# Kernel optimization log

Measured on AMD Instinct MI355X. Metric: run time of the kernel, lower is better.

The kernel has to match this reference:

```python
import jax, jax.numpy as jnp
import numpy as np

EPS = 1e-6
NUM_ITERS = 3


def rmsnorm(x, w, eps=EPS):
    # Qwen3RMSNorm: x * rsqrt(mean(x^2) + eps) * weight
    return x * jax.lax.rsqrt(jnp.mean(x * x, axis=-1, keepdims=True) + eps) * w


def setup_inputs() -> dict:
    key = jax.random.key(0)
    ks = jax.random.split(key, 12)
    B, K, M, d = 8, 64, 4096, 1024
    s = 0.02  # keep projections at sane init scale
    return {
        "slots": jax.random.normal(ks[0], (B, K, d), jnp.float32),
        "P": jax.random.normal(ks[1], (B, M, d), jnp.float32),
        "Wq": jax.random.normal(ks[2], (d, d), jnp.float32) * s,
        "Wk": jax.random.normal(ks[3], (d, d), jnp.float32) * s,
        "Wv": jax.random.normal(ks[4], (d, d), jnp.float32) * s,
        "gru_wi": jax.random.normal(ks[5], (3 * d, d), jnp.float32) * s,
        "gru_wh": jax.random.normal(ks[6], (3 * d, d), jnp.float32) * s,
        "gru_bi": jax.random.normal(ks[7], (3 * d,), jnp.float32) * s,
        "gru_bh": jax.random.normal(ks[8], (3 * d,), jnp.float32) * s,
        "slot_norm_w": jnp.ones((d,), jnp.float32),
        "input_norm_w": jnp.ones((d,), jnp.float32),
    }


def gru_cell(x, h, wi, wh, bi, bh):
    # PyTorch nn.GRUCell semantics; x,h: (..., d)
    d = h.shape[-1]
    gi = jnp.einsum('...d,ed->...e', x, wi) + bi  # (..., 3d)
    gh = jnp.einsum('...d,ed->...e', h, wh) + bh
    ir, iz, inn = gi[..., :d], gi[..., d:2 * d], gi[..., 2 * d:]
    hr, hz, hn = gh[..., :d], gh[..., d:2 * d], gh[..., 2 * d:]
    r = jax.nn.sigmoid(ir + hr)
    z = jax.nn.sigmoid(iz + hz)
    n = jnp.tanh(inn + r * hn)
    return (1.0 - z) * n + z * h


def reference(slots, P, Wq, Wk, Wv, gru_wi, gru_wh, gru_bi, gru_bh,
              slot_norm_w, input_norm_w):
    d = slots.shape[-1]
    scale = d ** (-0.5)
    Pn = rmsnorm(P, input_norm_w)
    k_proj = jnp.einsum('bmd,ed->bme', Pn, Wk)  # Linear: x @ W.T
    v_proj = jnp.einsum('bmd,ed->bme', Pn, Wv)
    for _ in range(NUM_ITERS):
        sn = rmsnorm(slots, slot_norm_w)
        q = jnp.einsum('bkd,ed->bke', sn, Wq)
        scores = jnp.einsum('bkd,bmd->bkm', q, k_proj) * scale
        attn = jax.nn.softmax(scores, axis=-2)  # softmax over SLOT axis K
        attn = attn / (jnp.sum(attn, axis=-1, keepdims=True) + EPS)
        updates = jnp.einsum('bkm,bmd->bkd', attn, v_proj)
        slots = gru_cell(updates, slots, gru_wi, gru_wh, gru_bi, gru_bh)
    return slots
```

## Files before the change

### kernel.cpp

```cpp
#include <hip/hip_runtime.h>

typedef __attribute__((ext_vector_type(4))) float f32x4;
typedef __attribute__((ext_vector_type(8))) short s16x8;

static __device__ __forceinline__ unsigned short f2bf(float f) {
  unsigned int u = __builtin_bit_cast(unsigned int, f);
  u += 0x7fffu + ((u >> 16) & 1u);
  return (unsigned short)(u >> 16);
}
static __device__ __forceinline__ float bf2f(unsigned short u) {
  return __builtin_bit_cast(float, (unsigned int)u << 16);
}
static __device__ __forceinline__ float sigm(float x) { return 1.0f / (1.0f + __expf(-x)); }

static __device__ __forceinline__ void gload16(const unsigned short* g, unsigned short* l) {
  __builtin_amdgcn_global_load_lds(
      (const __attribute__((address_space(1))) void*)g,
      (__attribute__((address_space(3))) void*)l, 16, 0, 0);
}

__global__ __launch_bounds__(256) void rmsnorm_k(const float* __restrict__ x,
                                                 const float* __restrict__ w,
                                                 unsigned short* __restrict__ y,
                                                 unsigned short* __restrict__ y_raw) {
  const int row = blockIdx.x;
  const int tid = threadIdx.x;
  const float4* xp = (const float4*)(x + (long)row * 1024);
  float4 v = xp[tid];
  float ss = v.x * v.x + v.y * v.y + v.z * v.z + v.w * v.w;
  #pragma unroll
  for (int off = 32; off; off >>= 1) ss += __shfl_xor(ss, off, 64);
  __shared__ float sb[4];
  if ((tid & 63) == 0) sb[tid >> 6] = ss;
  __syncthreads();
  float tot = sb[0] + sb[1] + sb[2] + sb[3];
  float rs = rsqrtf(tot * (1.0f / 1024.0f) + 1e-6f);
  const float4* wp = (const float4*)w;
  float4 wv = wp[tid];
  ushort4 o;
  o.x = f2bf(v.x * rs * wv.x);
  o.y = f2bf(v.y * rs * wv.y);
  o.z = f2bf(v.z * rs * wv.z);
  o.w = f2bf(v.w * rs * wv.w);
  ((ushort4*)y)[(long)row * 256 + tid] = o;
  if (y_raw) {
    ushort4 r;
    r.x = f2bf(v.x); r.y = f2bf(v.y); r.z = f2bf(v.z); r.w = f2bf(v.w);
    ((ushort4*)y_raw)[(long)row * 256 + tid] = r;
  }
}

__global__ __launch_bounds__(256) void tp_k(const unsigned short* __restrict__ in,
                                            unsigned short* __restrict__ out) {
  __shared__ unsigned short t[64][65];
  const int x = blockIdx.x;
  const int b = x >> 10;
  const int mt = (x & 1023) >> 4;
  const int dt = x & 15;
  const int tid = threadIdx.x;
  const long ibase = (long)b * 4096 * 1024 + (long)mt * 64 * 1024 + dt * 64;
  #pragma unroll
  for (int i = 0; i < 4; i++) {
    int idx = tid + i * 256;
    int r = idx >> 4, c4 = (idx & 15) * 4;
    ushort4 v = *(const ushort4*)(in + ibase + (long)r * 1024 + c4);
    t[r][c4] = v.x; t[r][c4 + 1] = v.y; t[r][c4 + 2] = v.z; t[r][c4 + 3] = v.w;
  }
  __syncthreads();
  const long obase = (long)b * 1024 * 4096 + (long)dt * 64 * 4096 + mt * 64;
  #pragma unroll
  for (int i = 0; i < 4; i++) {
    int idx = tid + i * 256;
    int r = idx >> 4, c4 = (idx & 15) * 4;
    ushort4 o;
    o.x = t[c4][r]; o.y = t[c4 + 1][r]; o.z = t[c4 + 2][r]; o.w = t[c4 + 3][r];
    *(ushort4*)(out + obase + (long)r * 4096 + c4) = o;
  }
}

static __device__ __forceinline__ void cvt_chunk(const float* __restrict__ in,
                                                 unsigned short* __restrict__ out, long i) {
  const float4* p = (const float4*)in;
  float4 a = p[i * 2], b = p[i * 2 + 1];
  ushort4 lo, hi;
  lo.x = f2bf(a.x); lo.y = f2bf(a.y); lo.z = f2bf(a.z); lo.w = f2bf(a.w);
  hi.x = f2bf(b.x); hi.y = f2bf(b.y); hi.z = f2bf(b.z); hi.w = f2bf(b.w);
  ushort4* o = (ushort4*)out;
  o[i * 2] = lo;
  o[i * 2 + 1] = hi;
}

__global__ __launch_bounds__(256) void prep_k(
    const float* __restrict__ Wq, const float* __restrict__ Wk, const float* __restrict__ Wv,
    const float* __restrict__ wi, const float* __restrict__ wh,
    const float* __restrict__ slots_in, const float* __restrict__ snw,
    unsigned short* __restrict__ wqt, unsigned short* __restrict__ wkt,
    unsigned short* __restrict__ wvt, unsigned short* __restrict__ wi_b,
    unsigned short* __restrict__ wh_b, unsigned short* __restrict__ sn,
    unsigned short* __restrict__ slotsb) {
  __shared__ float tile[64][65];
  const int x = blockIdx.x;
  const int tid = threadIdx.x;
  if (x < 768) {
    const int z = x >> 8, t = x & 255;
    const float* in = (z == 0) ? Wq : (z == 1) ? Wk : Wv;
    unsigned short* out = (z == 0) ? wqt : (z == 1) ? wkt : wvt;
    const int r0 = (t >> 4) * 64, c0 = (t & 15) * 64;
    #pragma unroll
    for (int i = 0; i < 4; i++) {
      int idx = tid + i * 256;
      int r = idx >> 4, c4 = (idx & 15) * 4;
      float4 v = *(const float4*)(in + (long)(r0 + r) * 1024 + c0 + c4);
      tile[r][c4] = v.x; tile[r][c4 + 1] = v.y; tile[r][c4 + 2] = v.z; tile[r][c4 + 3] = v.w;
    }
    __syncthreads();
    #pragma unroll
    for (int i = 0; i < 4; i++) {
      int idx = tid + i * 256;
      int c = idx >> 4, r4 = (idx & 15) * 4;
      ushort4 o;
      o.x = f2bf(tile[r4][c]);     o.y = f2bf(tile[r4 + 1][c]);
      o.z = f2bf(tile[r4 + 2][c]); o.w = f2bf(tile[r4 + 3][c]);
      *(ushort4*)(out + (long)(c0 + c) * 1024 + r0 + r4) = o;
    }
  } else if (x < 3840) {
    const int y = x - 768;
    if (y < 1536) cvt_chunk(wi, wi_b, (long)y * 256 + tid);
    else          cvt_chunk(wh, wh_b, (long)(y - 1536) * 256 + tid);
  } else {
    const int row = x - 3840;
    const float4* xp = (const float4*)(slots_in + (long)row * 1024);
    float4 v = xp[tid];
    float ss = v.x * v.x + v.y * v.y + v.z * v.z + v.w * v.w;
    #pragma unroll
    for (int off = 32; off; off >>= 1) ss += __shfl_xor(ss, off, 64);
    float* sb = &tile[0][0];
    if ((tid & 63) == 0) sb[tid >> 6] = ss;
    __syncthreads();
    float tot = sb[0] + sb[1] + sb[2] + sb[3];
    float rs = rsqrtf(tot * (1.0f / 1024.0f) + 1e-6f);
    float4 wv = ((const float4*)snw)[tid];
    ushort4 o;
    o.x = f2bf(v.x * rs * wv.x); o.y = f2bf(v.y * rs * wv.y);
    o.z = f2bf(v.z * rs * wv.z); o.w = f2bf(v.w * rs * wv.w);
    ((ushort4*)sn)[(long)row * 256 + tid] = o;
    ushort4 r;
    r.x = f2bf(v.x); r.y = f2bf(v.y); r.z = f2bf(v.z); r.w = f2bf(v.w);
    ((ushort4*)slotsb)[(long)row * 256 + tid] = r;
  }
}

template <int BM, int BN, int WR, int WC, typename CT, int EPI, int SPLIT, int QGH>
__global__ __launch_bounds__(WR * WC * 64) void gemm_bt(
    const unsigned short* __restrict__ A, const unsigned short* __restrict__ W,
    CT* __restrict__ C, int N, int Klen, int lda, int ldw,
    long sA, long sW, long sC, const float* __restrict__ bias,
    const float* __restrict__ bias2, float alpha, float* __restrict__ rs_part,
    const unsigned short* __restrict__ A2, const unsigned short* __restrict__ W2) {
  constexpr int BK = 64;
  constexpr int NT = WR * WC * 64;
  static_assert(NT == 256, "256 threads");
  constexpr int WSM = BM / WR, WSN = BN / WC;
  constexpr int MR = WSM / 16, NR = WSN / 16;
  constexpr int SEG_A = BM / 8, SEG_W = BN / 8;
  constexpr int PA = SEG_A / 4, PW = SEG_W / 4;
  static_assert(SEG_A % 4 == 0 && SEG_W % 4 == 0, "seg divisibility");
  __shared__ unsigned short As[BM * BK];
  __shared__ unsigned short Ws[BN * BK];
  const int tid = threadIdx.x, lane = tid & 63, wid = tid >> 6;
  const int wr = wid / WC, wc = wid % WC;
  const int tileN = blockIdx.x * BN, tileM = blockIdx.y * BM;
  int coff = 0;
  int zb = 0;
  if constexpr (QGH) {
    const int zz = blockIdx.z;
    if (zz > 0) {
      A = A2;
      W = W2 + (long)(zz - 1) * 1024 * ldw;
      bias = bias2 + (zz - 1) * 1024;
      coff = zz * 1024;
    }
  } else {
    zb = blockIdx.z / SPLIT;
    const int zs = blockIdx.z % SPLIT;
    A += (long)zb * sA + (long)zs * Klen;
    W += (long)zb * sW + (long)zs * Klen;
    C += (long)blockIdx.z * sC;
  }
  const int srow = lane >> 3;
  const int scol = (lane & 7) * 8;
  f32x4 acc[MR][NR];
  #pragma unroll
  for (int i = 0; i < MR; i++)
    #pragma unroll
    for (int j = 0; j < NR; j++) acc[i][j] = (f32x4){0.f, 0.f, 0.f, 0.f};
  const int fr = lane & 15, fq = lane >> 4;

  for (int k0 = 0; k0 < Klen; k0 += BK) {
    #pragma unroll
    for (int p = 0; p < PA; p++) {
      int seg = wid * PA + p;
      gload16(A + (long)(tileM + seg * 8 + srow) * lda + k0 + scol, &As[seg * 512]);
    }
    #pragma unroll
    for (int p = 0; p < PW; p++) {
      int seg = wid * PW + p;
      gload16(W + (long)(tileN + seg * 8 + srow) * ldw + k0 + scol, &Ws[seg * 512]);
    }
    __syncthreads();
    #pragma unroll
    for (int kk = 0; kk < BK; kk += 32) {
      s16x8 af[MR], bf[NR];
      #pragma unroll
      for (int i = 0; i < MR; i++)
        af[i] = *(const s16x8*)(&As[(wr * WSM + i * 16 + fr) * BK + kk + fq * 8]);
      #pragma unroll
      for (int j = 0; j < NR; j++)
        bf[j] = *(const s16x8*)(&Ws[(wc * WSN + j * 16 + fr) * BK + kk + fq * 8]);
      #pragma unroll
      for (int i = 0; i < MR; i++)
        #pragma unroll
        for (int j = 0; j < NR; j++)
          acc[i][j] = __builtin_amdgcn_mfma_f32_16x16x32_bf16(af[i], bf[j], acc[i][j], 0, 0, 0);
    }
    __syncthreads();
  }

  if constexpr (EPI == 2) {
    static_assert(WR == 1 && BM == 64, "softmax epilogue needs full-M wave");
    #pragma unroll
    for (int i = 0; i < MR; i++)
      #pragma unroll
      for (int j = 0; j < NR; j++)
        #pragma unroll
        for (int q = 0; q < 4; q++) acc[i][j][q] *= alpha;
    float inv[NR];
    #pragma unroll
    for (int j = 0; j < NR; j++) {
      float mx = -1e30f;
      #pragma unroll
      for (int i = 0; i < MR; i++)
        #pragma unroll
        for (int q = 0; q < 4; q++) mx = fmaxf(mx, acc[i][j][q]);
      mx = fmaxf(mx, __shfl_xor(mx, 16, 64));
      mx = fmaxf(mx, __shfl_xor(mx, 32, 64));
      float sm = 0.f;
      #pragma unroll
      for (int i = 0; i < MR; i++)
        #pragma unroll
        for (int q = 0; q < 4; q++) {
          float e = __expf(acc[i][j][q] - mx);
          acc[i][j][q] = e;
          sm += e;
        }
      sm += __shfl_xor(sm, 16, 64);
      sm += __shfl_xor(sm, 32, 64);
      inv[j] = 1.f / sm;
    }
    float rp[MR][4];
    #pragma unroll
    for (int i = 0; i < MR; i++)
      #pragma unroll
      for (int q = 0; q < 4; q++) rp[i][q] = 0.f;
    unsigned short* Cs = (unsigned short*)C;
    #pragma unroll
    for (int i = 0; i < MR; i++)
      #pragma unroll
      for (int j = 0; j < NR; j++)
        #pragma unroll
        for (int q = 0; q < 4; q++) {
          float a = acc[i][j][q] * inv[j];
          rp[i][q] += a;
          Cs[(long)(i * 16 + fq * 4 + q) * N + tileN + wc * WSN + j * 16 + fr] = f2bf(a);
        }
    #pragma unroll
    for (int off = 1; off <= 8; off <<= 1)
      #pragma unroll
      for (int i = 0; i < MR; i++)
        #pragma unroll
        for (int q = 0; q < 4; q++) rp[i][q] += __shfl_xor(rp[i][q], off, 64);
    if (fr == 0) {
      const int rld = gridDim.x * WC;
      #pragma unroll
      for (int i = 0; i < MR; i++)
        #pragma unroll
        for (int q = 0; q < 4; q++)
          rs_part[((long)zb * 64 + i * 16 + fq * 4 + q) * rld + blockIdx.x * WC + wc] = rp[i][q];
    }
    return;
  }

  #pragma unroll
  for (int i = 0; i < MR; i++) {
    const int mbase = tileM + wr * WSM + i * 16 + fq * 4;
    #pragma unroll
    for (int j = 0; j < NR; j++) {
      const int n = tileN + wc * WSN + j * 16 + fr;
      const float bv = bias ? bias[n] : 0.f;
      #pragma unroll
      for (int q = 0; q < 4; q++) {
        float v = acc[i][j][q] * alpha + bv;
        if constexpr (sizeof(CT) == 2)
          C[(long)(mbase + q) * N + coff + n] = f2bf(v);
        else
          C[(long)(mbase + q) * N + coff + n] = v;
      }
    }
  }
}

__global__ __launch_bounds__(256) void upd_reduce_k(const unsigned short* __restrict__ part,
                                                    const float* __restrict__ rs_part,
                                                    unsigned short* __restrict__ out) {
  const int row = blockIdx.x;
  const int tid = threadIdx.x;
  float s = rs_part[(long)row * 256 + tid];
  #pragma unroll
  for (int off = 32; off; off >>= 1) s += __shfl_xor(s, off, 64);
  __shared__ float sb[4];
  if ((tid & 63) == 0) sb[tid >> 6] = s;
  __syncthreads();
  const float inv = 1.f / (sb[0] + sb[1] + sb[2] + sb[3] + 1e-6f);
  const unsigned short* base =
      part + (long)(row >> 6) * 8 * 65536 + (long)(row & 63) * 1024 + tid * 4;
  float ax = 0.f, ay = 0.f, az = 0.f, aw = 0.f;
  #pragma unroll
  for (int sp = 0; sp < 8; sp++) {
    ushort4 v = *(const ushort4*)(base + (long)sp * 65536);
    ax += bf2f(v.x); ay += bf2f(v.y); az += bf2f(v.z); aw += bf2f(v.w);
  }
  ushort4 o;
  o.x = f2bf(ax * inv); o.y = f2bf(ay * inv);
  o.z = f2bf(az * inv); o.w = f2bf(aw * inv);
  ((ushort4*)out)[(long)row * 256 + tid] = o;
}

__global__ __launch_bounds__(256) void gru_k(const unsigned short* __restrict__ gi,
                                             const unsigned short* __restrict__ qgh,
                                             const float* __restrict__ h,
                                             const float* __restrict__ snw,
                                             float* __restrict__ out,
                                             unsigned short* __restrict__ out_bf,
                                             unsigned short* __restrict__ sn_out) {
  const int r = blockIdx.x;
  const int tid = threadIdx.x;
  const int c = tid * 4;
  const unsigned short* gip = gi + (long)r * 3072;
  const unsigned short* ghp = qgh + (long)r * 4096 + 1024;
  ushort4 iru = *(const ushort4*)(gip + c);
  ushort4 izu = *(const ushort4*)(gip + 1024 + c);
  ushort4 inu = *(const ushort4*)(gip + 2048 + c);
  ushort4 hru = *(const ushort4*)(ghp + c);
  ushort4 hzu = *(const ushort4*)(ghp + 1024 + c);
  ushort4 hnu = *(const ushort4*)(ghp + 2048 + c);
  float4 hv = *(const float4*)(h + (long)r * 1024 + c);
  float4 o;
  { float rr = sigm(bf2f(iru.x) + bf2f(hru.x)), zz = sigm(bf2f(izu.x) + bf2f(hzu.x));
    float nn = tanhf(bf2f(inu.x) + rr * bf2f(hnu.x)); o.x = (1.f - zz) * nn + zz * hv.x; }
  { float rr = sigm(bf2f(iru.y) + bf2f(hru.y)), zz = sigm(bf2f(izu.y) + bf2f(hzu.y));
    float nn = tanhf(bf2f(inu.y) + rr * bf2f(hnu.y)); o.y = (1.f - zz) * nn + zz * hv.y; }
  { float rr = sigm(bf2f(iru.z) + bf2f(hru.z)), zz = sigm(bf2f(izu.z) + bf2f(hzu.z));
    float nn = tanhf(bf2f(inu.z) + rr * bf2f(hnu.z)); o.z = (1.f - zz) * nn + zz * hv.z; }
  { float rr = sigm(bf2f(iru.w) + bf2f(hru.w)), zz = sigm(bf2f(izu.w) + bf2f(hzu.w));
    float nn = tanhf(bf2f(inu.w) + rr * bf2f(hnu.w)); o.w = (1.f - zz) * nn + zz * hv.w; }
  *(float4*)(out + (long)r * 1024 + c) = o;
  ushort4 ob;
  ob.x = f2bf(o.x); ob.y = f2bf(o.y); ob.z = f2bf(o.z); ob.w = f2bf(o.w);
  *(ushort4*)(out_bf + (long)r * 1024 + c) = ob;
  float ss = o.x * o.x + o.y * o.y + o.z * o.z + o.w * o.w;
  #pragma unroll
  for (int off = 32; off; off >>= 1) ss += __shfl_xor(ss, off, 64);
  __shared__ float sb[4];
  if ((tid & 63) == 0) sb[tid >> 6] = ss;
  __syncthreads();
  const float tot = sb[0] + sb[1] + sb[2] + sb[3];
  const float rs = rsqrtf(tot * (1.0f / 1024.0f) + 1e-6f);
  float4 wv = *(const float4*)(snw + c);
  ushort4 so;
  so.x = f2bf(o.x * rs * wv.x); so.y = f2bf(o.y * rs * wv.y);
  so.z = f2bf(o.z * rs * wv.z); so.w = f2bf(o.w * rs * wv.w);
  *(ushort4*)(sn_out + (long)r * 1024 + c) = so;
}

extern "C" void kernel_launch(void* const* d_in, const int* in_sizes, int n_in,
                              void* d_out, int out_size, void* d_ws, size_t ws_size,
                              hipStream_t stream) {
  const float* slots_in = (const float*)d_in[0];
  const float* P        = (const float*)d_in[1];
  const float* Wq       = (const float*)d_in[2];
  const float* Wk       = (const float*)d_in[3];
  const float* Wv       = (const float*)d_in[4];
  const float* wi       = (const float*)d_in[5];
  const float* wh       = (const float*)d_in[6];
  const float* bi       = (const float*)d_in[7];
  const float* bh       = (const float*)d_in[8];
  const float* snw      = (const float*)d_in[9];
  const float* inw      = (const float*)d_in[10];

  const size_t MB = 1024ull * 1024ull;
  char* ws = (char*)d_ws;
  unsigned short* Pn    = (unsigned short*)(ws + 0);
  unsigned short* Pnt   = (unsigned short*)(ws + 64 * MB);
  char* S               = ws + 128 * MB;
  unsigned short* sn    = (unsigned short*)(S);
  unsigned short* qgh   = (unsigned short*)(S + 1 * MB);
  unsigned short* attnb = (unsigned short*)(S + 5 * MB);
  unsigned short* updb  = (unsigned short*)(S + 9 * MB);
  unsigned short* slotsb= (unsigned short*)(S + 10 * MB);
  unsigned short* gi_b  = (unsigned short*)(S + 11 * MB);
  unsigned short* Cpart = (unsigned short*)(S + 14 * MB);
  float* rs_part        = (float*)(S + 22 * MB);
  unsigned short* wi_b  = (unsigned short*)(S + 23 * MB);
  unsigned short* wh_b  = (unsigned short*)(S + 29 * MB);
  unsigned short* wqt   = (unsigned short*)(S + 35 * MB);
  unsigned short* wkt   = (unsigned short*)(S + 37 * MB);
  unsigned short* wvt   = (unsigned short*)(S + 39 * MB);
  unsigned short* m1_b  = (unsigned short*)(S + 41 * MB);
  unsigned short* m2_b  = (unsigned short*)(S + 43 * MB);
  float* slots          = (float*)(ws + 196 * MB);

  prep_k<<<4352, 256, 0, stream>>>(Wq, Wk, Wv, wi, wh, slots_in, snw,
                                   wqt, wkt, wvt, wi_b, wh_b, sn, slotsb);
  rmsnorm_k<<<32768, 256, 0, stream>>>(P, inw, Pn, nullptr);
  tp_k<<<8192, 256, 0, stream>>>(Pn, Pnt);
  gemm_bt<64, 64, 2, 2, unsigned short, 0, 1, 0>
      <<<dim3(16, 16, 1), 256, 0, stream>>>(wkt, wqt, m1_b, 1024, 1024, 1024, 1024,
                                            0, 0, 0, nullptr, nullptr, 1.f, nullptr,
                                            nullptr, nullptr);
  gemm_bt<64, 64, 2, 2, unsigned short, 0, 1, 0>
      <<<dim3(16, 48, 1), 256, 0, stream>>>(wi_b, wvt, m2_b, 1024, 1024, 1024, 1024,
                                            0, 0, 0, nullptr, nullptr, 1.f, nullptr,
                                            nullptr, nullptr);

  for (int it = 0; it < 3; ++it) {
    gemm_bt<64, 64, 2, 2, unsigned short, 0, 1, 1>
        <<<dim3(16, 8, 4), 256, 0, stream>>>(sn, m1_b, qgh, 4096, 1024, 1024, 1024,
                                             0, 0, 0, nullptr, bh, 1.f, nullptr,
                                             slotsb, wh_b);
    gemm_bt<64, 64, 1, 4, unsigned short, 2, 1, 0>
        <<<dim3(64, 1, 8), 256, 0, stream>>>(qgh, Pn, attnb, 4096, 1024, 4096, 1024,
                                             64L * 4096, 4096L * 1024, 64L * 4096,
                                             nullptr, nullptr, 0.03125f, rs_part,
                                             nullptr, nullptr);
    gemm_bt<64, 64, 2, 2, unsigned short, 0, 8, 0>
        <<<dim3(16, 1, 64), 256, 0, stream>>>(attnb, Pnt, Cpart, 1024, 512, 4096, 4096,
                                              64L * 4096, 1024L * 4096, 64L * 1024,
                                              nullptr, nullptr, 1.f, nullptr,
                                              nullptr, nullptr);
    upd_reduce_k<<<512, 256, 0, stream>>>(Cpart, rs_part, updb);
    gemm_bt<64, 64, 2, 2, unsigned short, 0, 1, 0>
        <<<dim3(48, 8, 1), 256, 0, stream>>>(updb, m2_b, gi_b, 3072, 1024, 1024, 1024,
                                             0, 0, 0, bi, nullptr, 1.f, nullptr,
                                             nullptr, nullptr);
    const float* hsrc = (it == 0) ? slots_in : slots;
    float* dst = (it == 2) ? (float*)d_out : slots;
    gru_k<<<512, 256, 0, stream>>>(gi_b, qgh, hsrc, snw, dst, slotsb, sn);
  }
}
```

Measured before the change: 348.7 us.

## Fuse P rmsnorm with transpose and merge two weight-precompute GEMMs

Replaces the separate rmsnorm and transpose kernels with one kernel per 64-row tile. It computes row norms, writes normalized bf16 Pn, and transposes through LDS to Pnt, which removes a full re-read of Pn from global memory. It also merges the two weight-product GEMMs (Wk·Wq and Wi·Wv) into one launch by reordering the workspace so wkt and wi_b are contiguous, switching W to wvt for y>=16. The fused kernel launches only 512 blocks and reads P twice with serial loops, so it may have less parallelism and latency hiding.

```diff
diff --git a/kernel.cpp b/kernel.cpp
--- a/kernel.cpp
+++ b/kernel.cpp
@@ -19,62 +19,60 @@
       (__attribute__((address_space(3))) void*)l, 16, 0, 0);
 }
 
-__global__ __launch_bounds__(256) void rmsnorm_k(const float* __restrict__ x,
-                                                 const float* __restrict__ w,
-                                                 unsigned short* __restrict__ y,
-                                                 unsigned short* __restrict__ y_raw) {
-  const int row = blockIdx.x;
-  const int tid = threadIdx.x;
-  const float4* xp = (const float4*)(x + (long)row * 1024);
-  float4 v = xp[tid];
-  float ss = v.x * v.x + v.y * v.y + v.z * v.z + v.w * v.w;
-  #pragma unroll
-  for (int off = 32; off; off >>= 1) ss += __shfl_xor(ss, off, 64);
-  __shared__ float sb[4];
-  if ((tid & 63) == 0) sb[tid >> 6] = ss;
+__global__ __launch_bounds__(256) void rmstp_k(const float* __restrict__ P,
+                                               const float* __restrict__ inw,
+                                               unsigned short* __restrict__ Pn,
+                                               unsigned short* __restrict__ Pnt) {
+  __shared__ float psum[64][4];
+  __shared__ float rinv[64];
+  __shared__ float winw[1024];
+  __shared__ unsigned short tile[64][65];
+  const int blk = blockIdx.x;
+  const int b = blk >> 6, mt = blk & 63;
+  const int tid = threadIdx.x, lane = tid & 63, wid = tid >> 6;
+  const float* base = P + ((long)b * 4096 + (long)mt * 64) * 1024;
+  {
+    float4 w4 = ((const float4*)inw)[tid];
+    *(float4*)(&winw[tid * 4]) = w4;
+  }
+  for (int r = 0; r < 64; r++) {
+    float4 v = ((const float4*)(base + (long)r * 1024))[tid];
+    float ss = v.x * v.x + v.y * v.y + v.z * v.z + v.w * v.w;
+    #pragma unroll
+    for (int off = 32; off; off >>= 1) ss += __shfl_xor(ss, off, 64);
+    if (lane == 0) psum[r][wid] = ss;
+  }
   __syncthreads();
-  float tot = sb[0] + sb[1] + sb[2] + sb[3];
-  float rs = rsqrtf(tot * (1.0f / 1024.0f) + 1e-6f);
-  const float4* wp = (const float4*)w;
-  float4 wv = wp[tid];
-  ushort4 o;
-  o.x = f2bf(v.x * rs * wv.x);
-  o.y = f2bf(v.y * rs * wv.y);
-  o.z = f2bf(v.z * rs * wv.z);
-  o.w = f2bf(v.w * rs * wv.w);
-  ((ushort4*)y)[(long)row * 256 + tid] = o;
-  if (y_raw) {
-    ushort4 r;
-    r.x = f2bf(v.x); r.y = f2bf(v.y); r.z = f2bf(v.z); r.w = f2bf(v.w);
-    ((ushort4*)y_raw)[(long)row * 256 + tid] = r;
-  }
-}
-
-__global__ __launch_bounds__(256) void tp_k(const unsigned short* __restrict__ in,
-                                            unsigned short* __restrict__ out) {
-  __shared__ unsigned short t[64][65];
-  const int x = blockIdx.x;
-  const int b = x >> 10;
-  const int mt = (x & 1023) >> 4;
-  const int dt = x & 15;
-  const int tid = threadIdx.x;
-  const long ibase = (long)b * 4096 * 1024 + (long)mt * 64 * 1024 + dt * 64;
-  #pragma unroll
-  for (int i = 0; i < 4; i++) {
-    int idx = tid + i * 256;
-    int r = idx >> 4, c4 = (idx & 15) * 4;
-    ushort4 v = *(const ushort4*)(in + ibase + (long)r * 1024 + c4);
-    t[r][c4] = v.x; t[r][c4 + 1] = v.y; t[r][c4 + 2] = v.z; t[r][c4 + 3] = v.w;
+  if (tid < 64) {
+    float tot = psum[tid][0] + psum[tid][1] + psum[tid][2] + psum[tid][3];
+    rinv[tid] = rsqrtf(tot * (1.0f / 1024.0f) + 1e-6f);
   }
   __syncthreads();
-  const long obase = (long)b * 1024 * 4096 + (long)dt * 64 * 4096 + mt * 64;
-  #pragma unroll
-  for (int i = 0; i < 4; i++) {
-    int idx = tid + i * 256;
-    int r = idx >> 4, c4 = (idx & 15) * 4;
-    ushort4 o;
-    o.x = t[c4][r]; o.y = t[c4 + 1][r]; o.z = t[c4 + 2][r]; o.w = t[c4 + 3][r];
-    *(ushort4*)(out + obase + (long)r * 4096 + c4) = o;
+  const int rr = tid >> 4;
+  const int c4 = (tid & 15) * 4;
+  for (int dt = 0; dt < 16; dt++) {
+    #pragma unroll
+    for (int i = 0; i < 4; i++) {
+      int r = i * 16 + rr;
+      float4 v = *(const float4*)(base + (long)r * 1024 + dt * 64 + c4);
+      float rs = rinv[r];
+      ushort4 o;
+      o.x = f2bf(v.x * rs * winw[dt * 64 + c4]);
+      o.y = f2bf(v.y * rs * winw[dt * 64 + c4 + 1]);
+      o.z = f2bf(v.z * rs * winw[dt * 64 + c4 + 2]);
+      o.w = f2bf(v.w * rs * winw[dt * 64 + c4 + 3]);
+      *(ushort4*)(Pn + ((long)b * 4096 + mt * 64 + r) * 1024 + dt * 64 + c4) = o;
+      tile[r][c4] = o.x; tile[r][c4 + 1] = o.y; tile[r][c4 + 2] = o.z; tile[r][c4 + 3] = o.w;
+    }
+    __syncthreads();
+    #pragma unroll
+    for (int i = 0; i < 4; i++) {
+      int c = i * 16 + rr;
+      ushort4 o;
+      o.x = tile[c4][c]; o.y = tile[c4 + 1][c]; o.z = tile[c4 + 2][c]; o.w = tile[c4 + 3][c];
+      *(ushort4*)(Pnt + ((long)b * 1024 + dt * 64 + c) * 4096 + (long)mt * 64 + c4) = o;
+    }
+    __syncthreads();
   }
 }
 
@@ -150,7 +148,7 @@
   }
 }
 
-template <int BM, int BN, int WR, int WC, typename CT, int EPI, int SPLIT, int QGH>
+template <int BM, int BN, int WR, int WC, typename CT, int EPI, int SPLIT, int QGH, int M12>
 __global__ __launch_bounds__(WR * WC * 64) void gemm_bt(
     const unsigned short* __restrict__ A, const unsigned short* __restrict__ W,
     CT* __restrict__ C, int N, int Klen, int lda, int ldw,
@@ -180,6 +178,8 @@
       bias = bias2 + (zz - 1) * 1024;
       coff = zz * 1024;
     }
+  } else if constexpr (M12) {
+    if (blockIdx.y >= 16) W = W2;
   } else {
     zb = blockIdx.z / SPLIT;
     const int zs = blockIdx.z % SPLIT;
@@ -410,45 +410,40 @@
   unsigned short* gi_b  = (unsigned short*)(S + 11 * MB);
   unsigned short* Cpart = (unsigned short*)(S + 14 * MB);
   float* rs_part        = (float*)(S + 22 * MB);
-  unsigned short* wi_b  = (unsigned short*)(S + 23 * MB);
-  unsigned short* wh_b  = (unsigned short*)(S + 29 * MB);
-  unsigned short* wqt   = (unsigned short*)(S + 35 * MB);
-  unsigned short* wkt   = (unsigned short*)(S + 37 * MB);
-  unsigned short* wvt   = (unsigned short*)(S + 39 * MB);
+  unsigned short* wqt   = (unsigned short*)(S + 23 * MB);
+  unsigned short* wvt   = (unsigned short*)(S + 25 * MB);
+  unsigned short* wh_b  = (unsigned short*)(S + 27 * MB);
+  unsigned short* wkt   = (unsigned short*)(S + 33 * MB);
+  unsigned short* wi_b  = (unsigned short*)(S + 35 * MB);
   unsigned short* m1_b  = (unsigned short*)(S + 41 * MB);
   unsigned short* m2_b  = (unsigned short*)(S + 43 * MB);
   float* slots          = (float*)(ws + 196 * MB);
 
   prep_k<<<4352, 256, 0, stream>>>(Wq, Wk, Wv, wi, wh, slots_in, snw,
                                    wqt, wkt, wvt, wi_b, wh_b, sn, slotsb);
-  rmsnorm_k<<<32768, 256, 0, stream>>>(P, inw, Pn, nullptr);
-  tp_k<<<8192, 256, 0, stream>>>(Pn, Pnt);
-  gemm_bt<64, 64, 2, 2, unsigned short, 0, 1, 0>
-      <<<dim3(16, 16, 1), 256, 0, stream>>>(wkt, wqt, m1_b, 1024, 1024, 1024, 1024,
+  rmstp_k<<<512, 256, 0, stream>>>(P, inw, Pn, Pnt);
+  gemm_bt<64, 64, 2, 2, unsigned short, 0, 1, 0, 1>
+      <<<dim3(16, 64, 1), 256, 0, stream>>>(wkt, wqt, m1_b, 1024, 1024, 1024, 1024,
                                             0, 0, 0, nullptr, nullptr, 1.f, nullptr,
-                                            nullptr, nullptr);
-  gemm_bt<64, 64, 2, 2, unsigned short, 0, 1, 0>
-      <<<dim3(16, 48, 1), 256, 0, stream>>>(wi_b, wvt, m2_b, 1024, 1024, 1024, 1024,
-                                            0, 0, 0, nullptr, nullptr, 1.f, nullptr,
-                                            nullptr, nullptr);
+                                            nullptr, wvt);
 
   for (int it = 0; it < 3; ++it) {
-    gemm_bt<64, 64, 2, 2, unsigned short, 0, 1, 1>
+    gemm_bt<64, 64, 2, 2, unsigned short, 0, 1, 1, 0>
         <<<dim3(16, 8, 4), 256, 0, stream>>>(sn, m1_b, qgh, 4096, 1024, 1024, 1024,
                                              0, 0, 0, nullptr, bh, 1.f, nullptr,
                                              slotsb, wh_b);
-    gemm_bt<64, 64, 1, 4, unsigned short, 2, 1, 0>
+    gemm_bt<64, 64, 1, 4, unsigned short, 2, 1, 0, 0>
         <<<dim3(64, 1, 8), 256, 0, stream>>>(qgh, Pn, attnb, 4096, 1024, 4096, 1024,
                                              64L * 4096, 4096L * 1024, 64L * 4096,
                                              nullptr, nullptr, 0.03125f, rs_part,
                                              nullptr, nullptr);
-    gemm_bt<64, 64, 2, 2, unsigned short, 0, 8, 0>
+    gemm_bt<64, 64, 2, 2, unsigned short, 0, 8, 0, 0>
         <<<dim3(16, 1, 64), 256, 0, stream>>>(attnb, Pnt, Cpart, 1024, 512, 4096, 4096,
                                               64L * 4096, 1024L * 4096, 64L * 1024,
                                               nullptr, nullptr, 1.f, nullptr,
                                               nullptr, nullptr);
     upd_reduce_k<<<512, 256, 0, stream>>>(Cpart, rs_part, updb);
-    gemm_bt<64, 64, 2, 2, unsigned short, 0, 1, 0>
+    gemm_bt<64, 64, 2, 2, unsigned short, 0, 1, 0, 0>
         <<<dim3(48, 8, 1), 256, 0, stream>>>(updb, m2_b, gi_b, 3072, 1024, 1024, 1024,
                                              0, 0, 0, bi, nullptr, 1.f, nullptr,
                                              nullptr, nullptr);
```

Measured after the change: 371.7 us. 1.07x slower.
